# Kernel optimization log

Hardware: AMD Instinct MI355X
Metric: run time of the kernel (lower is better)

The kernel has to match this reference:

```python
import jax, jax.numpy as jnp
import numpy as np

B, V, D = 8, 2048, 3
CL1_F, CL1_K = 64, 6
CL2_F, CL2_K = 128, 5
F1, F2 = 512, 256


def _uniform(k, shape, fin, fout):
    s = np.sqrt(2.0 / (fin + fout)).astype(np.float32)
    return jax.random.uniform(k, shape, jnp.float32, -s, s)


def setup_inputs() -> dict:
    key = jax.random.key(0)
    ks = jax.random.split(key, 8)
    x = jax.random.normal(ks[0], (B, D, V), jnp.float32)
    # dense stand-in for the scaled graph Laplacian; scaled so spectral radius < 1
    L = jax.random.normal(ks[1], (B, V, V), jnp.float32) * (0.5 / np.sqrt(V))
    L = 0.5 * (L + L.transpose(0, 2, 1))  # symmetric like a real Laplacian
    return {
        "x": x,
        "L": L,
        "cl1_w": _uniform(ks[2], (CL1_F, D * CL1_K), CL1_K, CL1_F),
        "cl1_b": jnp.zeros((CL1_F,), jnp.float32),
        "cl2_w": _uniform(ks[3], (CL2_F, CL2_K * CL1_F), CL2_K * CL1_F, CL2_F),
        "cl2_b": jnp.zeros((CL2_F,), jnp.float32),
        "fc1_w": _uniform(ks[4], (F1, CL2_F), CL2_F, F1),
        "fc1_b": jnp.zeros((F1,), jnp.float32),
        "fc2_w": _uniform(ks[5], (F2, F1), F1, F2),
        "fc2_b": jnp.zeros((F2,), jnp.float32),
    }


def _cheby_conv(x, L, W, b, K):
    # x: [B, V, Fin], L: [B, V, V] -> [B, V, Fout]
    x0 = x
    xs = [x0]
    if K > 1:
        x1 = jnp.einsum('bvu,buf->bvf', L, x0)
        xs.append(x1)
    for _ in range(2, K):
        x2 = 2.0 * jnp.einsum('bvu,buf->bvf', L, x1) - x0
        xs.append(x2)
        x0, x1 = x1, x2
    # torch ordering: feature index = fin * K + k  -> stack K on last axis
    xk = jnp.stack(xs, axis=-1)                 # [B, V, Fin, K]
    xk = xk.reshape(xk.shape[0], xk.shape[1], -1)  # [B, V, Fin*K]
    return xk @ W.T + b


def reference(x, L, cl1_w, cl1_b, cl2_w, cl2_b, fc1_w, fc1_b, fc2_w, fc2_b):
    xp = x.transpose(0, 2, 1)                    # [B, V, D]
    y = jax.nn.relu(_cheby_conv(xp, L, cl1_w, cl1_b, CL1_K))
    y = jax.nn.relu(_cheby_conv(y, L, cl2_w, cl2_b, CL2_K))
    y = jax.nn.relu(y @ fc1_w.T + fc1_b)
    y = jax.nn.relu(y @ fc2_w.T + fc2_b)
    return y                                     # [B, V, F2]
```

## Files before the change

### kernel.cpp

```cpp
#include <hip/hip_runtime.h>

#define B_ 8
#define V_ 2048
#define D_ 3
#define M_ (B_*V_)

typedef __attribute__((ext_vector_type(8))) short short8;
typedef __attribute__((ext_vector_type(4))) float f32x4;

__device__ inline void async_copy16(const void* g, void* lds) {
  __builtin_amdgcn_global_load_lds(
      (const __attribute__((address_space(1))) unsigned int*)g,
      (__attribute__((address_space(3))) unsigned int*)lds, 16, 0, 0);
}

__device__ inline void split_bf16(float v, short& hi, short& lo) {
  unsigned u  = __float_as_uint(v);
  unsigned hb = u & 0xFFFF0000u;
  float d = v - __uint_as_float(hb);
  hi = (short)(hb >> 16);
  lo = (short)(__float_as_uint(d) >> 16);
}

__global__ __launch_bounds__(256) void k_prep(
    const float* __restrict__ x,
    const float* __restrict__ w1, const float* __restrict__ w2,
    const float* __restrict__ fw1, const float* __restrict__ fw2,
    float* __restrict__ xa,
    short* __restrict__ XKh, short* __restrict__ XKl,
    short* __restrict__ w1h, short* __restrict__ w1l,
    short* __restrict__ w2h, short* __restrict__ w2l,
    short* __restrict__ fw1h, short* __restrict__ fw1l,
    short* __restrict__ fw2h, short* __restrict__ fw2l) {
  int i = blockIdx.x * 256 + threadIdx.x;
  short hi, lo;
  if (i < M_*64) {
    int r = i >> 6, s = i & 63;
    float val = 0.f;
    if (s == 0 || s == 6 || s == 12) {
      int f = s / 6;
      int b = r >> 11, v = r & (V_-1);
      val = x[((size_t)b*D_ + f)*V_ + v];
      xa[(size_t)r*3 + f] = val;
    }
    split_bf16(val, hi, lo);
    XKh[i] = hi; XKl[i] = lo;
    return;
  }
  i -= M_*64;
  if (i < 4096) {
    int n = i >> 6, k = i & 63;
    float v = (k < 18) ? w1[n*18 + k] : 0.f;
    split_bf16(v, hi, lo); w1h[i] = hi; w1l[i] = lo; return;
  }
  i -= 4096;
  if (i < 40960) { split_bf16(w2[i],  hi, lo); w2h[i]=hi;  w2l[i]=lo;  return; }
  i -= 40960;
  if (i < 65536) { split_bf16(fw1[i], hi, lo); fw1h[i]=hi; fw1l[i]=lo; return; }
  i -= 65536;
  if (i < 131072){ split_bf16(fw2[i], hi, lo); fw2h[i]=hi; fw2l[i]=lo; return; }
}

__global__ __launch_bounds__(256) void k_cheby1(const float* __restrict__ L,
    const float* __restrict__ xc, const float* __restrict__ xp,
    float* __restrict__ xn, short* __restrict__ XKh, short* __restrict__ XKl,
    float alpha, float beta, int kidx) {
  __shared__ float sx[3][V_];
  int b  = blockIdx.x >> 8;
  int r0 = (blockIdx.x & 255) * 8;
  const float* xcb = xc + (size_t)b*V_*D_;
  for (int i = threadIdx.x; i < V_*D_; i += 256) {
    int u = i / 3, f = i - u*3;
    sx[f][u] = xcb[i];
  }
  __syncthreads();
  int w = threadIdx.x >> 6, lane = threadIdx.x & 63;
  const float4* X0 = (const float4*)sx[0];
  const float4* X1 = (const float4*)sx[1];
  const float4* X2 = (const float4*)sx[2];
  int rA = r0 + w*2;
  int rB = rA + 1;
  const float4* LA = (const float4*)(L + ((size_t)b*V_ + rA)*V_);
  const float4* LB = (const float4*)(L + ((size_t)b*V_ + rB)*V_);
  float a0=0.f,a1=0.f,a2=0.f,b0=0.f,b1=0.f,b2=0.f;
  #pragma unroll
  for (int it = 0; it < 8; it++) {
    int u4 = it*64 + lane;
    float4 la = LA[u4], lb = LB[u4];
    float4 x0 = X0[u4], x1 = X1[u4], x2 = X2[u4];
    a0 = fmaf(la.x,x0.x,fmaf(la.y,x0.y,fmaf(la.z,x0.z,fmaf(la.w,x0.w,a0))));
    a1 = fmaf(la.x,x1.x,fmaf(la.y,x1.y,fmaf(la.z,x1.z,fmaf(la.w,x1.w,a1))));
    a2 = fmaf(la.x,x2.x,fmaf(la.y,x2.y,fmaf(la.z,x2.z,fmaf(la.w,x2.w,a2))));
    b0 = fmaf(lb.x,x0.x,fmaf(lb.y,x0.y,fmaf(lb.z,x0.z,fmaf(lb.w,x0.w,b0))));
    b1 = fmaf(lb.x,x1.x,fmaf(lb.y,x1.y,fmaf(lb.z,x1.z,fmaf(lb.w,x1.w,b1))));
    b2 = fmaf(lb.x,x2.x,fmaf(lb.y,x2.y,fmaf(lb.z,x2.z,fmaf(lb.w,x2.w,b2))));
  }
  #pragma unroll
  for (int off = 32; off > 0; off >>= 1) {
    a0 += __shfl_down(a0, off); a1 += __shfl_down(a1, off);
    a2 += __shfl_down(a2, off); b0 += __shfl_down(b0, off);
    b1 += __shfl_down(b1, off); b2 += __shfl_down(b2, off);
  }
  if (lane == 0) {
    float vA[3] = {alpha*a0, alpha*a1, alpha*a2};
    float vB[3] = {alpha*b0, alpha*b1, alpha*b2};
    size_t baseA = ((size_t)b*V_ + rA)*3;
    size_t baseB = ((size_t)b*V_ + rB)*3;
    if (beta != 0.f) {
      #pragma unroll
      for (int f = 0; f < 3; f++) {
        vA[f] -= beta * xp[baseA + f];
        vB[f] -= beta * xp[baseB + f];
      }
    }
    #pragma unroll
    for (int f = 0; f < 3; f++) {
      xn[baseA + f] = vA[f];
      xn[baseB + f] = vB[f];
      short hi, lo;
      split_bf16(vA[f], hi, lo);
      size_t oA = ((size_t)b*V_ + rA)*64 + f*6 + kidx;
      XKh[oA] = hi; XKl[oA] = lo;
      split_bf16(vB[f], hi, lo);
      size_t oB = ((size_t)b*V_ + rB)*64 + f*6 + kidx;
      XKh[oB] = hi; XKl[oB] = lo;
    }
  }
}

__global__ __launch_bounds__(256) void k_cheby2_mfma(const float* __restrict__ L,
    const short* __restrict__ Zth, const short* __restrict__ Ztl,
    const float* __restrict__ Zp,
    float* __restrict__ Zn, short* __restrict__ ZKh, short* __restrict__ ZKl,
    short* __restrict__ Znth, short* __restrict__ Zntl,
    float alpha, float beta, int kidx) {
  __shared__ float sA[16*64];
  __shared__ short sBh[64*64];
  __shared__ short sBl[64*64];

  int b  = blockIdx.x >> 7;
  int r0 = (blockIdx.x & 127) * 16;
  const float* Lb   = L   + (size_t)b*V_*V_;
  const short* Zthb = Zth + (size_t)b*64*V_;
  const short* Ztlb = Ztl + (size_t)b*64*V_;

  int tid  = threadIdx.x;
  int w    = tid >> 6;
  int lane = tid & 63;
  int lm   = lane & 15;
  int quad = lane >> 4;
  int cbase = w * 16;

  const f32x4*  sAv  = (const f32x4*)sA;
  const short8* sBhv = (const short8*)sBh;
  const short8* sBlv = (const short8*)sBl;

  f32x4 acc = {0.f,0.f,0.f,0.f};

  for (int s = 0; s < V_/64; s++) {
    int k0 = s * 64;
    if (s) __syncthreads();
    {
      int f = tid;
      int r = f >> 4, cc = f & 15;
      int c = cc ^ r;
      async_copy16(Lb + (size_t)(r0 + r)*V_ + k0 + c*4, &sA[f*4]);
    }
    #pragma unroll
    for (int t = 0; t < 2; t++) {
      int f = t*256 + tid;
      int n = f >> 3, cc = f & 7;
      int c = cc ^ (n & 7);
      async_copy16(Zthb + (size_t)n*V_ + k0 + c*8, &sBh[f*8]);
      async_copy16(Ztlb + (size_t)n*V_ + k0 + c*8, &sBl[f*8]);
    }
    __syncthreads();

    #pragma unroll
    for (int ks = 0; ks < 2; ks++) {
      int koff = ks * 32;
      int r = lm;
      int c0 = (koff >> 2) + 2*quad;
      f32x4 a0 = sAv[r*16 + (c0 ^ r)];
      f32x4 a1 = sAv[r*16 + ((c0 + 1) ^ r)];
      float av[8] = {a0.x, a0.y, a0.z, a0.w, a1.x, a1.y, a1.z, a1.w};
      short8 ah, al;
      #pragma unroll
      for (int j = 0; j < 8; j++) {
        short hi, lo; split_bf16(av[j], hi, lo);
        ah[j] = hi; al[j] = lo;
      }
      int cb = (koff >> 3) + quad;
      int n = cbase + lm;
      short8 bh = sBhv[n*8 + (cb ^ (n & 7))];
      short8 bl = sBlv[n*8 + (cb ^ (n & 7))];
      acc = __builtin_amdgcn_mfma_f32_16x16x32_bf16(ah, bh, acc, 0, 0, 0);
      acc = __builtin_amdgcn_mfma_f32_16x16x32_bf16(ah, bl, acc, 0, 0, 0);
      acc = __builtin_amdgcn_mfma_f32_16x16x32_bf16(al, bh, acc, 0, 0, 0);
    }
  }

  int n = cbase + lm;
  #pragma unroll
  for (int i = 0; i < 4; i++) {
    int r = r0 + quad*4 + i;
    size_t rowb = (size_t)b*V_ + r;
    float v = alpha * acc[i];
    if (beta != 0.f) v -= beta * Zp[rowb*64 + n];
    Zn[rowb*64 + n] = v;
    short hi, lo; split_bf16(v, hi, lo);
    size_t ok = rowb*320 + (size_t)n*5 + kidx;
    ZKh[ok] = hi; ZKl[ok] = lo;
    size_t o = ((size_t)b*64 + n)*V_ + r;
    Znth[o] = hi; Zntl[o] = lo;
  }
}

__device__ __forceinline__ void gemm_tile(
    const short* __restrict__ Ah, const short* __restrict__ Al,
    const short* __restrict__ Wh, const short* __restrict__ Wl,
    const float* __restrict__ bias, int N, int K, int row0, int col0,
    short* sAh, short* sAl, short* sWh, short* sWl,
    float* __restrict__ Cf, short* __restrict__ Ch, short* __restrict__ Cl,
    short* __restrict__ Ph, short* __restrict__ Pl, int packMul, int packStride,
    short* __restrict__ Th, short* __restrict__ Tl) {
  int tid = threadIdx.x, w = tid >> 6, lane = tid & 63;
  int lm = lane & 15, quad = lane >> 4;
  int wm = (w & 1) * 32, wn = (w >> 1) * 32;

  const short8* vAh = (const short8*)sAh;
  const short8* vAl = (const short8*)sAl;
  const short8* vWh = (const short8*)sWh;
  const short8* vWl = (const short8*)sWl;

  f32x4 acc[2][2] = {{{0.f,0.f,0.f,0.f},{0.f,0.f,0.f,0.f}},
                     {{0.f,0.f,0.f,0.f},{0.f,0.f,0.f,0.f}}};

  for (int k0 = 0; k0 < K; k0 += 64) {
    if (k0) __syncthreads();
    #pragma unroll
    for (int t = 0; t < 2; t++) {
      int f = t*256 + tid;
      int r = f >> 3, p = f & 7;
      int c = p ^ (r & 7);
      size_t goA = (size_t)(row0 + r)*K + k0 + c*8;
      size_t goW = (size_t)(col0 + r)*K + k0 + c*8;
      async_copy16(Ah + goA, &sAh[f*8]);
      async_copy16(Al + goA, &sAl[f*8]);
      async_copy16(Wh + goW, &sWh[f*8]);
      async_copy16(Wl + goW, &sWl[f*8]);
    }
    __syncthreads();

    #pragma unroll
    for (int ks = 0; ks < 2; ks++) {
      int kc = ks*4 + quad;
      short8 a_h[2], a_l[2], b_h[2], b_l[2];
      #pragma unroll
      for (int i = 0; i < 2; i++) {
        int m = wm + i*16 + lm;
        a_h[i] = vAh[m*8 + (kc ^ (m & 7))];
        a_l[i] = vAl[m*8 + (kc ^ (m & 7))];
      }
      #pragma unroll
      for (int j = 0; j < 2; j++) {
        int n = wn + j*16 + lm;
        b_h[j] = vWh[n*8 + (kc ^ (n & 7))];
        b_l[j] = vWl[n*8 + (kc ^ (n & 7))];
      }
      #pragma unroll
      for (int i = 0; i < 2; i++)
        #pragma unroll
        for (int j = 0; j < 2; j++) {
          acc[i][j] = __builtin_amdgcn_mfma_f32_16x16x32_bf16(a_h[i], b_h[j], acc[i][j], 0, 0, 0);
          acc[i][j] = __builtin_amdgcn_mfma_f32_16x16x32_bf16(a_h[i], b_l[j], acc[i][j], 0, 0, 0);
          acc[i][j] = __builtin_amdgcn_mfma_f32_16x16x32_bf16(a_l[i], b_h[j], acc[i][j], 0, 0, 0);
        }
    }
  }

  #pragma unroll
  for (int i = 0; i < 2; i++)
    #pragma unroll
    for (int j = 0; j < 2; j++) {
      int col = col0 + wn + j*16 + lm;
      float bj = bias[col];
      #pragma unroll
      for (int g = 0; g < 4; g++) {
        int row = row0 + wm + i*16 + quad*4 + g;
        float v = acc[i][j][g] + bj;
        v = v > 0.f ? v : 0.f;
        if (Cf) Cf[(size_t)row*N + col] = v;
        short hi, lo;
        if (Ch || Ph || Th) split_bf16(v, hi, lo);
        if (Ch) {
          Ch[(size_t)row*N + col] = hi;
          Cl[(size_t)row*N + col] = lo;
        }
        if (Ph) {
          size_t o = (size_t)row*packStride + (size_t)col*packMul;
          Ph[o] = hi; Pl[o] = lo;
        }
        if (Th) {
          int bb = row >> 11, vv = row & (V_-1);
          size_t o = ((size_t)bb*64 + col)*V_ + vv;
          Th[o] = hi; Tl[o] = lo;
        }
      }
    }
}

__global__ __launch_bounds__(256) void k_gemm_y1(
    const short* __restrict__ XKh, const short* __restrict__ XKl,
    const short* __restrict__ w1h, const short* __restrict__ w1l,
    const float* __restrict__ b1, float* __restrict__ y1,
    short* __restrict__ ZKh, short* __restrict__ ZKl,
    short* __restrict__ Th, short* __restrict__ Tl) {
  __shared__ short sAh[64*64], sAl[64*64], sWh[64*64], sWl[64*64];
  gemm_tile(XKh, XKl, w1h, w1l, b1, 64, 64, blockIdx.x*64, 0,
            sAh, sAl, sWh, sWl,
            y1, nullptr, nullptr, ZKh, ZKl, 5, 320, Th, Tl);
}

__global__ __launch_bounds__(256) void k_gemm_bf16(
    const short* __restrict__ Ah, const short* __restrict__ Al,
    const short* __restrict__ Wh, const short* __restrict__ Wl,
    const float* __restrict__ bias, int N, int K,
    float* __restrict__ Cf, short* __restrict__ Ch, short* __restrict__ Cl) {
  __shared__ short sAh[64*64], sAl[64*64], sWh[64*64], sWl[64*64];
  int bm = blockIdx.x & 255;
  int bn = blockIdx.x >> 8;
  gemm_tile(Ah, Al, Wh, Wl, bias, N, K, bm*64, bn*64,
            sAh, sAl, sWh, sWl,
            Cf, Ch, Cl, nullptr, nullptr, 0, 0, nullptr, nullptr);
}

extern "C" void kernel_launch(void* const* d_in, const int* in_sizes, int n_in,
                              void* d_out, int out_size, void* d_ws, size_t ws_size,
                              hipStream_t stream) {
  const float* x   = (const float*)d_in[0];
  const float* L   = (const float*)d_in[1];
  const float* w1  = (const float*)d_in[2];
  const float* b1  = (const float*)d_in[3];
  const float* w2  = (const float*)d_in[4];
  const float* b2  = (const float*)d_in[5];
  const float* fw1 = (const float*)d_in[6];
  const float* fb1 = (const float*)d_in[7];
  const float* fw2 = (const float*)d_in[8];
  const float* fb2 = (const float*)d_in[9];
  float* out = (float*)d_out;

  float* p  = (float*)d_ws;
  float* xa = p;  p += (size_t)B_*V_*D_;
  float* xb = p;  p += (size_t)B_*V_*D_;
  float* xc = p;  p += (size_t)B_*V_*D_;
  float* y1 = p;  p += (size_t)M_*64;
  float* zb = p;  p += (size_t)M_*64;
  float* zc = p;  p += (size_t)M_*64;
  short* sp = (short*)p;
  short* ZKh = sp;  sp += (size_t)M_*320;
  short* ZKl = sp;  sp += (size_t)M_*320;
  short* y2h = sp;  sp += (size_t)M_*128;
  short* y2l = sp;  sp += (size_t)M_*128;
  short* h1h = sp;  sp += (size_t)M_*512;
  short* h1l = sp;  sp += (size_t)M_*512;
  short* ZtAh = sp; sp += (size_t)M_*64;
  short* ZtAl = sp; sp += (size_t)M_*64;
  short* ZtBh = sp; sp += (size_t)M_*64;
  short* ZtBl = sp; sp += (size_t)M_*64;
  short* w1h = sp;  sp += 64*64;
  short* w1l = sp;  sp += 64*64;
  short* w2h = sp;  sp += 128*320;
  short* w2l = sp;  sp += 128*320;
  short* fw1h = sp; sp += 512*128;
  short* fw1l = sp; sp += 512*128;
  short* fw2h = sp; sp += 256*512;
  short* fw2l = sp; sp += 256*512;
  short* XKh = h1h;
  short* XKl = h1h + (size_t)M_*64;

  k_prep<<<5040, 256, 0, stream>>>(x, w1, w2, fw1, fw2, xa,
                                   XKh, XKl, w1h, w1l, w2h, w2l,
                                   fw1h, fw1l, fw2h, fw2l);

  k_cheby1<<<2048, 256, 0, stream>>>(L, xa, xa, xb, XKh, XKl, 1.f, 0.f, 1);
  k_cheby1<<<2048, 256, 0, stream>>>(L, xb, xa, xc, XKh, XKl, 2.f, 1.f, 2);
  k_cheby1<<<2048, 256, 0, stream>>>(L, xc, xb, xa, XKh, XKl, 2.f, 1.f, 3);
  k_cheby1<<<2048, 256, 0, stream>>>(L, xa, xc, xb, XKh, XKl, 2.f, 1.f, 4);
  k_cheby1<<<2048, 256, 0, stream>>>(L, xb, xa, xc, XKh, XKl, 2.f, 1.f, 5);

  k_gemm_y1<<<256, 256, 0, stream>>>(XKh, XKl, w1h, w1l, b1,
                                     y1, ZKh, ZKl, ZtAh, ZtAl);

  k_cheby2_mfma<<<1024, 256, 0, stream>>>(L, ZtAh, ZtAl, y1, zb, ZKh, ZKl,
                                          ZtBh, ZtBl, 1.f, 0.f, 1);
  k_cheby2_mfma<<<1024, 256, 0, stream>>>(L, ZtBh, ZtBl, y1, zc, ZKh, ZKl,
                                          ZtAh, ZtAl, 2.f, 1.f, 2);
  k_cheby2_mfma<<<1024, 256, 0, stream>>>(L, ZtAh, ZtAl, zb, y1, ZKh, ZKl,
                                          ZtBh, ZtBl, 2.f, 1.f, 3);
  k_cheby2_mfma<<<1024, 256, 0, stream>>>(L, ZtBh, ZtBl, zc, zb, ZKh, ZKl,
                                          ZtAh, ZtAl, 2.f, 1.f, 4);

  k_gemm_bf16<<<512, 256, 0, stream>>>(ZKh, ZKl, w2h, w2l, b2, 128, 320,
                                       nullptr, y2h, y2l);
  k_gemm_bf16<<<2048, 256, 0, stream>>>(y2h, y2l, fw1h, fw1l, fb1, 512, 128,
                                        nullptr, h1h, h1l);
  k_gemm_bf16<<<1024, 256, 0, stream>>>(h1h, h1l, fw2h, fw2l, fb2, 256, 512,
                                        out, nullptr, nullptr);
}
```

Baseline: 547.3 us.

## Double-buffer LDS staging in cheby2 MFMA and process four rows per warp in cheby1

The cheby2 MFMA kernel gets double-buffered shared memory, so the async global-to-LDS copy for the next K tile is issued before computing on the current one, with one barrier per iteration. The cheby1 kernel now has each warp handle four Laplacian rows instead of two, halving the grid and amortizing the per-block staging of x into LDS, and its epilogue uses vectorized float4 loads and stores. The intent is to hide load latency in the dominant L-streaming kernels and cut redundant LDS fills. The cost is twice the LDS in cheby2 and more registers in cheby1, which may lower occupancy.

After: 536.6 us. 2.0% less time.

```diff
diff --git a/kernel.cpp b/kernel.cpp
--- a/kernel.cpp
+++ b/kernel.cpp
@@ -66,8 +66,8 @@
     float* __restrict__ xn, short* __restrict__ XKh, short* __restrict__ XKl,
     float alpha, float beta, int kidx) {
   __shared__ float sx[3][V_];
-  int b  = blockIdx.x >> 8;
-  int r0 = (blockIdx.x & 255) * 8;
+  int b  = blockIdx.x >> 7;
+  int r0 = (blockIdx.x & 127) * 16;
   const float* xcb = xc + (size_t)b*V_*D_;
   for (int i = threadIdx.x; i < V_*D_; i += 256) {
     int u = i / 3, f = i - u*3;
@@ -78,53 +78,61 @@
   const float4* X0 = (const float4*)sx[0];
   const float4* X1 = (const float4*)sx[1];
   const float4* X2 = (const float4*)sx[2];
-  int rA = r0 + w*2;
-  int rB = rA + 1;
-  const float4* LA = (const float4*)(L + ((size_t)b*V_ + rA)*V_);
-  const float4* LB = (const float4*)(L + ((size_t)b*V_ + rB)*V_);
-  float a0=0.f,a1=0.f,a2=0.f,b0=0.f,b1=0.f,b2=0.f;
+  int rbase = r0 + w*4;
+  const float4* Lr[4];
   #pragma unroll
+  for (int rr = 0; rr < 4; rr++)
+    Lr[rr] = (const float4*)(L + ((size_t)b*V_ + rbase + rr)*V_);
+
+  float acc[4][3] = {{0.f,0.f,0.f},{0.f,0.f,0.f},{0.f,0.f,0.f},{0.f,0.f,0.f}};
+
+  #pragma unroll 2
   for (int it = 0; it < 8; it++) {
     int u4 = it*64 + lane;
-    float4 la = LA[u4], lb = LB[u4];
     float4 x0 = X0[u4], x1 = X1[u4], x2 = X2[u4];
-    a0 = fmaf(la.x,x0.x,fmaf(la.y,x0.y,fmaf(la.z,x0.z,fmaf(la.w,x0.w,a0))));
-    a1 = fmaf(la.x,x1.x,fmaf(la.y,x1.y,fmaf(la.z,x1.z,fmaf(la.w,x1.w,a1))));
-    a2 = fmaf(la.x,x2.x,fmaf(la.y,x2.y,fmaf(la.z,x2.z,fmaf(la.w,x2.w,a2))));
-    b0 = fmaf(lb.x,x0.x,fmaf(lb.y,x0.y,fmaf(lb.z,x0.z,fmaf(lb.w,x0.w,b0))));
-    b1 = fmaf(lb.x,x1.x,fmaf(lb.y,x1.y,fmaf(lb.z,x1.z,fmaf(lb.w,x1.w,b1))));
-    b2 = fmaf(lb.x,x2.x,fmaf(lb.y,x2.y,fmaf(lb.z,x2.z,fmaf(lb.w,x2.w,b2))));
+    #pragma unroll
+    for (int rr = 0; rr < 4; rr++) {
+      float4 lv = Lr[rr][u4];
+      acc[rr][0] = fmaf(lv.x,x0.x,fmaf(lv.y,x0.y,fmaf(lv.z,x0.z,fmaf(lv.w,x0.w,acc[rr][0]))));
+      acc[rr][1] = fmaf(lv.x,x1.x,fmaf(lv.y,x1.y,fmaf(lv.z,x1.z,fmaf(lv.w,x1.w,acc[rr][1]))));
+      acc[rr][2] = fmaf(lv.x,x2.x,fmaf(lv.y,x2.y,fmaf(lv.z,x2.z,fmaf(lv.w,x2.w,acc[rr][2]))));
+    }
   }
   #pragma unroll
-  for (int off = 32; off > 0; off >>= 1) {
-    a0 += __shfl_down(a0, off); a1 += __shfl_down(a1, off);
-    a2 += __shfl_down(a2, off); b0 += __shfl_down(b0, off);
-    b1 += __shfl_down(b1, off); b2 += __shfl_down(b2, off);
-  }
+  for (int off = 32; off > 0; off >>= 1)
+    #pragma unroll
+    for (int rr = 0; rr < 4; rr++)
+      #pragma unroll
+      for (int f = 0; f < 3; f++)
+        acc[rr][f] += __shfl_down(acc[rr][f], off);
+
   if (lane == 0) {
-    float vA[3] = {alpha*a0, alpha*a1, alpha*a2};
-    float vB[3] = {alpha*b0, alpha*b1, alpha*b2};
-    size_t baseA = ((size_t)b*V_ + rA)*3;
-    size_t baseB = ((size_t)b*V_ + rB)*3;
+    size_t base = ((size_t)b*V_ + rbase)*3;
+    float v[12];
+    #pragma unroll
+    for (int rr = 0; rr < 4; rr++)
+      #pragma unroll
+      for (int f = 0; f < 3; f++)
+        v[rr*3+f] = alpha*acc[rr][f];
     if (beta != 0.f) {
+      const float4* xp4 = (const float4*)(xp + base);
+      float4 p0 = xp4[0], p1 = xp4[1], p2 = xp4[2];
+      v[0] -= beta*p0.x; v[1]  -= beta*p0.y; v[2]  -= beta*p0.z; v[3]  -= beta*p0.w;
+      v[4] -= beta*p1.x; v[5]  -= beta*p1.y; v[6]  -= beta*p1.z; v[7]  -= beta*p1.w;
+      v[8] -= beta*p2.x; v[9]  -= beta*p2.y; v[10] -= beta*p2.z; v[11] -= beta*p2.w;
+    }
+    float4* xn4 = (float4*)(xn + base);
+    xn4[0] = make_float4(v[0], v[1], v[2],  v[3]);
+    xn4[1] = make_float4(v[4], v[5], v[6],  v[7]);
+    xn4[2] = make_float4(v[8], v[9], v[10], v[11]);
+    #pragma unroll
+    for (int rr = 0; rr < 4; rr++)
       #pragma unroll
       for (int f = 0; f < 3; f++) {
-        vA[f] -= beta * xp[baseA + f];
-        vB[f] -= beta * xp[baseB + f];
+        short hi, lo; split_bf16(v[rr*3+f], hi, lo);
+        size_t o = ((size_t)b*V_ + rbase + rr)*64 + f*6 + kidx;
+        XKh[o] = hi; XKl[o] = lo;
       }
-    }
-    #pragma unroll
-    for (int f = 0; f < 3; f++) {
-      xn[baseA + f] = vA[f];
-      xn[baseB + f] = vB[f];
-      short hi, lo;
-      split_bf16(vA[f], hi, lo);
-      size_t oA = ((size_t)b*V_ + rA)*64 + f*6 + kidx;
-      XKh[oA] = hi; XKl[oA] = lo;
-      split_bf16(vB[f], hi, lo);
-      size_t oB = ((size_t)b*V_ + rB)*64 + f*6 + kidx;
-      XKh[oB] = hi; XKl[oB] = lo;
-    }
   }
 }
 
@@ -134,9 +142,9 @@
     float* __restrict__ Zn, short* __restrict__ ZKh, short* __restrict__ ZKl,
     short* __restrict__ Znth, short* __restrict__ Zntl,
     float alpha, float beta, int kidx) {
-  __shared__ float sA[16*64];
-  __shared__ short sBh[64*64];
-  __shared__ short sBl[64*64];
+  __shared__ float sA[2][16*64];
+  __shared__ short sBh[2][64*64];
+  __shared__ short sBl[2][64*64];
 
   int b  = blockIdx.x >> 7;
   int r0 = (blockIdx.x & 127) * 16;
@@ -151,38 +159,45 @@
   int quad = lane >> 4;
   int cbase = w * 16;
 
-  const f32x4*  sAv  = (const f32x4*)sA;
-  const short8* sBhv = (const short8*)sBh;
-  const short8* sBlv = (const short8*)sBl;
+  int rS  = tid >> 4;
+  int cS  = (tid & 15) ^ rS;
+  size_t gA  = (size_t)(r0 + rS)*V_ + cS*4;
+  int nS0 = tid >> 3;
+  int cS0 = (tid & 7) ^ (nS0 & 7);
+  size_t gB0 = (size_t)nS0*V_ + cS0*8;
+  int fS1 = 256 + tid;
+  int nS1 = fS1 >> 3;
+  int cS1 = (fS1 & 7) ^ (nS1 & 7);
+  size_t gB1 = (size_t)nS1*V_ + cS1*8;
+
+  auto stage = [&](int bb, int k0) {
+    async_copy16(Lb   + gA  + k0, &sA[bb][tid*4]);
+    async_copy16(Zthb + gB0 + k0, &sBh[bb][tid*8]);
+    async_copy16(Ztlb + gB0 + k0, &sBl[bb][tid*8]);
+    async_copy16(Zthb + gB1 + k0, &sBh[bb][fS1*8]);
+    async_copy16(Ztlb + gB1 + k0, &sBl[bb][fS1*8]);
+  };
 
   f32x4 acc = {0.f,0.f,0.f,0.f};
 
+  stage(0, 0);
+  __syncthreads();
+
   for (int s = 0; s < V_/64; s++) {
-    int k0 = s * 64;
-    if (s) __syncthreads();
-    {
-      int f = tid;
-      int r = f >> 4, cc = f & 15;
-      int c = cc ^ r;
-      async_copy16(Lb + (size_t)(r0 + r)*V_ + k0 + c*4, &sA[f*4]);
-    }
-    #pragma unroll
-    for (int t = 0; t < 2; t++) {
-      int f = t*256 + tid;
-      int n = f >> 3, cc = f & 7;
-      int c = cc ^ (n & 7);
-      async_copy16(Zthb + (size_t)n*V_ + k0 + c*8, &sBh[f*8]);
-      async_copy16(Ztlb + (size_t)n*V_ + k0 + c*8, &sBl[f*8]);
-    }
-    __syncthreads();
+    int bb = s & 1;
+    if (s < V_/64 - 1) stage(bb ^ 1, (s+1)*64);
+
+    const f32x4*  sAv  = (const f32x4*)sA[bb];
+    const short8* sBhv = (const short8*)sBh[bb];
+    const short8* sBlv = (const short8*)sBl[bb];
 
     #pragma unroll
     for (int ks = 0; ks < 2; ks++) {
       int koff = ks * 32;
       int r = lm;
-      int c0 = (koff >> 2) + 2*quad;
-      f32x4 a0 = sAv[r*16 + (c0 ^ r)];
-      f32x4 a1 = sAv[r*16 + ((c0 + 1) ^ r)];
+      int ca = (koff >> 2) + 2*quad;
+      f32x4 a0 = sAv[r*16 + (ca ^ r)];
+      f32x4 a1 = sAv[r*16 + ((ca + 1) ^ r)];
       float av[8] = {a0.x, a0.y, a0.z, a0.w, a1.x, a1.y, a1.z, a1.w};
       short8 ah, al;
       #pragma unroll
@@ -198,6 +213,7 @@
       acc = __builtin_amdgcn_mfma_f32_16x16x32_bf16(ah, bl, acc, 0, 0, 0);
       acc = __builtin_amdgcn_mfma_f32_16x16x32_bf16(al, bh, acc, 0, 0, 0);
     }
+    __syncthreads();
   }
 
   int n = cbase + lm;
@@ -383,11 +399,11 @@
                                    XKh, XKl, w1h, w1l, w2h, w2l,
                                    fw1h, fw1l, fw2h, fw2l);
 
-  k_cheby1<<<2048, 256, 0, stream>>>(L, xa, xa, xb, XKh, XKl, 1.f, 0.f, 1);
-  k_cheby1<<<2048, 256, 0, stream>>>(L, xb, xa, xc, XKh, XKl, 2.f, 1.f, 2);
-  k_cheby1<<<2048, 256, 0, stream>>>(L, xc, xb, xa, XKh, XKl, 2.f, 1.f, 3);
-  k_cheby1<<<2048, 256, 0, stream>>>(L, xa, xc, xb, XKh, XKl, 2.f, 1.f, 4);
-  k_cheby1<<<2048, 256, 0, stream>>>(L, xb, xa, xc, XKh, XKl, 2.f, 1.f, 5);
+  k_cheby1<<<1024, 256, 0, stream>>>(L, xa, xa, xb, XKh, XKl, 1.f, 0.f, 1);
+  k_cheby1<<<1024, 256, 0, stream>>>(L, xb, xa, xc, XKh, XKl, 2.f, 1.f, 2);
+  k_cheby1<<<1024, 256, 0, stream>>>(L, xc, xb, xa, XKh, XKl, 2.f, 1.f, 3);
+  k_cheby1<<<1024, 256, 0, stream>>>(L, xa, xc, xb, XKh, XKl, 2.f, 1.f, 4);
+  k_cheby1<<<1024, 256, 0, stream>>>(L, xb, xa, xc, XKh, XKl, 2.f, 1.f, 5);
 
   k_gemm_y1<<<256, 256, 0, stream>>>(XKh, XKl, w1h, w1l, b1,
                                      y1, ZKh, ZKl, ZtAh, ZtAl);
```
